# Kernel tuning notes

Measured on AMD Instinct MI355X. Metric: run time of the kernel, lower is better.

The kernel has to match this reference:

```python
import jax, jax.numpy as jnp
import numpy as np

H, W = 256, 256
N = 512


def setup_inputs() -> dict:
    key = jax.random.key(0)
    k1, k2, k3, k4, k5 = jax.random.split(key, 5)
    # gaussian centers in front of the camera
    xy = jax.random.normal(k1, (N, 2), dtype=jnp.float32) * 3.0
    z = jax.random.uniform(k2, (N,), dtype=jnp.float32, minval=2.0, maxval=45.0)
    means3D = jnp.concatenate([xy, z[:, None]], axis=1)  # (N,3)
    # SPD 3x3 covariances
    A = jax.random.normal(k3, (N, 3, 3), dtype=jnp.float32) * 0.2
    covs3d = jnp.einsum('nij,nkj->nik', A, A) + 0.05 * jnp.eye(3, dtype=jnp.float32)
    colors = jax.random.uniform(k4, (N, 3), dtype=jnp.float32)
    opacities = jax.random.uniform(k5, (N,), dtype=jnp.float32)
    K = jnp.array([[300.0, 0.0, W / 2.0], [0.0, 300.0, H / 2.0], [0.0, 0.0, 1.0]], dtype=jnp.float32)
    R = jnp.eye(3, dtype=jnp.float32)
    t = jnp.zeros((3,), dtype=jnp.float32)
    return {"means3D": means3D, "covs3d": covs3d, "colors": colors,
            "opacities": opacities, "K": K, "R": R, "t": t}


def _render(means3D, covs3d, colors, opacities, K, R, t):
    # --- projection ---
    cam = means3D @ R.T + t                       # (N,3)
    Z = cam[:, 2]                                 # raw camera-space depth
    depths = jnp.maximum(Z, 1.0)                  # clamped (used for sort/mask)
    screen = cam @ K.T
    means2D = screen[:, :2] / screen[:, 2:3]      # (N,2)
    fx, fy = K[0, 0], K[1, 1]
    zeros = jnp.zeros_like(Z)
    # Jacobian of perspective projection, (N,2,3); uses raw Z as in the original
    J = jnp.stack([
        jnp.stack([fx / Z, zeros, -fx * cam[:, 0] / (Z * Z)], axis=-1),
        jnp.stack([zeros, fy / Z, -fy * cam[:, 1] / (Z * Z)], axis=-1),
    ], axis=1)
    covs_cam = jnp.einsum('ij,njk,lk->nil', R, covs3d, R)     # R Sigma R^T
    covs2D = jnp.einsum('nij,njk,nlk->nil', J, covs_cam, J)   # J Sigma_cam J^T, (N,2,2)

    valid = (depths > 1.0) & (depths < 50.0)
    # front-to-back sort by clamped depth
    idx = jnp.argsort(depths)
    means2D = means2D[idx]
    covs2D = covs2D[idx]
    colors_s = colors[idx]
    op_s = opacities[idx]
    valid = valid[idx]

    # --- per-gaussian per-pixel density ---
    covs2D = covs2D + 1e-4 * jnp.eye(2, dtype=covs2D.dtype)
    cov_inv = jnp.linalg.inv(covs2D)              # (N,2,2)
    cov_det = jnp.linalg.det(covs2D)              # (N,)
    norm = 1.0 / (2.0 * jnp.pi * jnp.sqrt(cov_det))

    ys, xs = jnp.meshgrid(jnp.arange(H, dtype=jnp.float32),
                          jnp.arange(W, dtype=jnp.float32), indexing='ij')
    pixels = jnp.stack([xs, ys], axis=-1)         # (H,W,2), [x,y]

    dx = pixels[None] - means2D[:, None, None, :]                 # (N,H,W,2)
    expo = -0.5 * jnp.einsum('nhwi,nij,nhwj->nhw', dx, cov_inv, dx)
    gaussian = norm[:, None, None] * jnp.exp(expo)                # (N,H,W)
    gaussian = gaussian * valid.astype(gaussian.dtype)[:, None, None]

    # --- alpha compositing (inclusive cumprod as in the original) ---
    alphas = op_s[:, None, None] * gaussian                       # (N,H,W)
    T = jnp.cumprod(1.0 - alphas, axis=0)
    weights = alphas * T
    rendered = jnp.einsum('nhw,nc->hwc', weights, colors_s)       # (H,W,3)
    return rendered


def reference(means3D, covs3d, colors, opacities, K, R, t):
    return _render(means3D, covs3d, colors, opacities, K, R, t)
```

## Files before the change

### kernel.cpp

```cpp
#include <hip/hip_runtime.h>


constexpr int   REC   = 16;
constexpr int   WIMG  = 256;
constexpr int   HIMG  = 256;
constexpr int   SPLIT = 8;
constexpr float LOG2E  = 1.4426950408889634f;
constexpr float INV2PI = 0.15915494309189535f;
constexpr float INVEPS = 1.0e7f;

__global__ __launch_bounds__(512) void gs_preprocess(
    const float* __restrict__ means3D, const float* __restrict__ covs3d,
    const float* __restrict__ colors,  const float* __restrict__ opac,
    const float* __restrict__ Km,      const float* __restrict__ Rm,
    const float* __restrict__ tvec,    float* __restrict__ recs, int N)
{
    __shared__ float s_depth[512];
    __shared__ int   s_cnt[64][9];
    const int t  = threadIdx.x;
    const int l  = t & 63, p = t >> 6;
    const int gi = (int)blockIdx.x * 64 + l;

    float d_all = 3.0e38f;
    if (t < N) {
        const float m0 = means3D[t*3+0], m1 = means3D[t*3+1], m2 = means3D[t*3+2];
        d_all = fmaxf(Rm[6]*m0 + Rm[7]*m1 + Rm[8]*m2 + tvec[2], 1.0f);
    }
    s_depth[t] = d_all;
    __syncthreads();

    const float dg = s_depth[gi & 511];
    int cnt = 0;
    #pragma unroll 16
    for (int j = p*64; j < p*64 + 64; ++j) {
        const float dj = s_depth[j];
        cnt += (dj < dg) || (dj == dg && j < gi);
    }
    s_cnt[l][p] = cnt;

    float rec[13];
    const bool act = (p == 0) && (gi < N);
    if (act) {
        float Kl[9], Rl[9], tl[3];
        #pragma unroll
        for (int k = 0; k < 9; ++k) { Kl[k] = Km[k]; Rl[k] = Rm[k]; }
        tl[0] = tvec[0]; tl[1] = tvec[1]; tl[2] = tvec[2];

        const float m0 = means3D[gi*3+0], m1 = means3D[gi*3+1], m2 = means3D[gi*3+2];
        const float cam0 = Rl[0]*m0 + Rl[1]*m1 + Rl[2]*m2 + tl[0];
        const float cam1 = Rl[3]*m0 + Rl[4]*m1 + Rl[5]*m2 + tl[1];
        const float cam2 = Rl[6]*m0 + Rl[7]*m1 + Rl[8]*m2 + tl[2];
        const float Z = cam2;
        const float depth = fmaxf(Z, 1.0f);

        const float s0 = Kl[0]*cam0 + Kl[1]*cam1 + Kl[2]*cam2;
        const float s1 = Kl[3]*cam0 + Kl[4]*cam1 + Kl[5]*cam2;
        const float s2 = Kl[6]*cam0 + Kl[7]*cam1 + Kl[8]*cam2;
        const float mx = s0 / s2, my = s1 / s2;

        const float fx = Kl[0], fy = Kl[4];
        const float iz = 1.0f / Z;
        float J[2][3];
        J[0][0] = fx*iz; J[0][1] = 0.0f;  J[0][2] = -fx*cam0*iz*iz;
        J[1][0] = 0.0f;  J[1][1] = fy*iz; J[1][2] = -fy*cam1*iz*iz;

        float S[9];
        #pragma unroll
        for (int k = 0; k < 9; ++k) S[k] = covs3d[gi*9+k];

        float RS[9], Cc[9];
        #pragma unroll
        for (int r = 0; r < 3; ++r)
            #pragma unroll
            for (int c = 0; c < 3; ++c)
                RS[r*3+c] = Rl[r*3+0]*S[0+c] + Rl[r*3+1]*S[3+c] + Rl[r*3+2]*S[6+c];
        #pragma unroll
        for (int r = 0; r < 3; ++r)
            #pragma unroll
            for (int c = 0; c < 3; ++c)
                Cc[r*3+c] = RS[r*3+0]*Rl[c*3+0] + RS[r*3+1]*Rl[c*3+1] + RS[r*3+2]*Rl[c*3+2];

        float JC[2][3];
        #pragma unroll
        for (int r = 0; r < 2; ++r)
            #pragma unroll
            for (int c = 0; c < 3; ++c)
                JC[r][c] = J[r][0]*Cc[0+c] + J[r][1]*Cc[3+c] + J[r][2]*Cc[6+c];

        const float c200 = JC[0][0]*J[0][0] + JC[0][1]*J[0][1] + JC[0][2]*J[0][2] + 1e-4f;
        const float c201 = JC[0][0]*J[1][0] + JC[0][1]*J[1][1] + JC[0][2]*J[1][2];
        const float c210 = JC[1][0]*J[0][0] + JC[1][1]*J[0][1] + JC[1][2]*J[0][2];
        const float c211 = JC[1][0]*J[1][0] + JC[1][1]*J[1][1] + JC[1][2]*J[1][2] + 1e-4f;

        const float det  = c200*c211 - c201*c210;
        const float idet = 1.0f / det;
        const float ia   = c211*idet;
        const float i01  = -0.5f*(c201 + c210)*idet;
        const float ic   = c200*idet;
        const float ibs  = 2.0f*i01;

        const bool  valid = (depth > 1.0f) && (depth < 50.0f);
        const float nrm   = valid ? (INV2PI / sqrtf(det)) : 0.0f;
        const float opn   = opac[gi] * nrm;

        const float c1 = i01 / ia;
        const float c2 = ic - i01*i01/ia;
        const float L2 = 2.0f * logf(opn * INVEPS);

        rec[0]  = my;  rec[1] = c2;  rec[2] = L2;  rec[3] = c1;
        rec[4]  = mx;  rec[5] = ia;
        rec[6]  = -0.5f*LOG2E*ia;
        rec[7]  = -0.5f*LOG2E*ibs;
        rec[8]  = -0.5f*LOG2E*ic;
        rec[9]  = opn;
        rec[10] = colors[gi*3+0];
        rec[11] = colors[gi*3+1];
        rec[12] = colors[gi*3+2];
    }
    __syncthreads();

    if (act) {
        int rank = 0;
        #pragma unroll
        for (int q = 0; q < 8; ++q) rank += s_cnt[l][q];
        float4* dst = (float4*)(recs + rank*REC);
        dst[0] = make_float4(rec[0],  rec[1],  rec[2],  rec[3]);
        dst[1] = make_float4(rec[4],  rec[5],  rec[6],  rec[7]);
        dst[2] = make_float4(rec[8],  rec[9],  rec[10], rec[11]);
        dst[3] = make_float4(rec[12], 0.0f,    0.0f,    0.0f);
    }
}

__global__ __launch_bounds__(512, 8) void gs_render(
    const float* __restrict__ recs, float* __restrict__ out, int N)
{
    __shared__ float  s_my[512], s_c2[512], s_L2[512], s_c1[512], s_mx[512], s_p0[512];
    __shared__ float  s_ev[512][12];
    __shared__ float4 s_part[SPLIT][64];
    __shared__ float  s_rgb[192];

    const int t = threadIdx.x;

    if (t < N) {
        const float4 a = *(const float4*)(recs + t*REC + 0);
        const float4 b = *(const float4*)(recs + t*REC + 4);
        const float4 c = *(const float4*)(recs + t*REC + 8);
        const float4 d = *(const float4*)(recs + t*REC + 12);
        s_my[t] = a.x; s_c2[t] = a.y; s_L2[t] = a.z; s_c1[t] = a.w;
        s_mx[t] = b.x; s_p0[t] = b.y;
        float4* ev = (float4*)s_ev[t];
        ev[0] = make_float4(b.x, a.x, b.z, b.w);
        ev[1] = make_float4(c.x, c.y, c.z, c.w);
        s_ev[t][8] = d.x;
    } else {
        s_my[t] = 0.0f; s_c2[t] = 0.0f; s_L2[t] = -1e30f;
        s_c1[t] = 0.0f; s_mx[t] = 0.0f; s_p0[t] = 1.0f;
    }
    __syncthreads();

    const int w    = t >> 6;
    const int lane = t & 63;
    const float sx0 = (float)(((int)blockIdx.x & 3) * 64);
    const float scx = sx0 + 31.5f;
    const float px  = sx0 + (float)lane;
    const float py  = (float)((int)blockIdx.x >> 2);

    const int base = w * 64;
    bool hit;
    {
        const int j = base + lane;
        const float dy  = py - s_my[j];
        const float rem = fmaf(-s_c2[j], dy*dy, s_L2[j]);
        const float xc  = fmaf(-s_c1[j], dy, s_mx[j]);
        const float t1  = fmaxf(fabsf(xc - scx) - 31.5f, 0.0f);
        hit = (s_p0[j]*t1*t1 <= rem);
    }
    unsigned long long mask = __ballot(hit);

    float T = 1.0f, cr = 0.0f, cg = 0.0f, cb = 0.0f;
    while (mask) {
        const int k = __builtin_ctzll(mask);
        mask &= mask - 1;
        const float* e = s_ev[base + k];
        const float4 v0 = *(const float4*)(e + 0);
        const float4 v1 = *(const float4*)(e + 4);
        const float  bl = e[8];
        const float dx = px - v0.x;
        const float dy = py - v0.y;
        const float e2 = fmaf(v0.z, dx*dx, fmaf(v0.w, dx*dy, v1.x*dy*dy));
        const float al = v1.y * __builtin_amdgcn_exp2f(e2);
        T *= (1.0f - al);
        const float wt = al * T;
        cr = fmaf(wt, v1.z, cr);
        cg = fmaf(wt, v1.w, cg);
        cb = fmaf(wt, bl,  cb);
    }

    s_part[w][lane] = make_float4(T, cr, cg, cb);
    __syncthreads();

    if (t < 64) {
        float4 f = s_part[0][t];
        float Ta = f.x, r_ = f.y, g_ = f.z, b_ = f.w;
        #pragma unroll
        for (int k = 1; k < SPLIT; ++k) {
            const float4 p = s_part[k][t];
            r_ = fmaf(Ta, p.y, r_);
            g_ = fmaf(Ta, p.z, g_);
            b_ = fmaf(Ta, p.w, b_);
            Ta *= p.x;
        }
        s_rgb[t*3+0] = r_;
        s_rgb[t*3+1] = g_;
        s_rgb[t*3+2] = b_;
    }
    __syncthreads();

    if (t < 192) {
        out[(int)blockIdx.x * 192 + t] = s_rgb[t];
    }
}

extern "C" void kernel_launch(void* const* d_in, const int* in_sizes, int n_in,
                              void* d_out, int out_size, void* d_ws, size_t ws_size,
                              hipStream_t stream)
{
    const float* means3D = (const float*)d_in[0];
    const float* covs3d  = (const float*)d_in[1];
    const float* colors  = (const float*)d_in[2];
    const float* opac    = (const float*)d_in[3];
    const float* Km      = (const float*)d_in[4];
    const float* Rm      = (const float*)d_in[5];
    const float* tv      = (const float*)d_in[6];
    const int N = in_sizes[3];

    float* recs = (float*)d_ws;
    float* out  = (float*)d_out;

    gs_preprocess<<<dim3((N + 63) / 64), dim3(512), 0, stream>>>(
        means3D, covs3d, colors, opac, Km, Rm, tv, recs, N);

    gs_render<<<dim3(WIMG * HIMG / 64), dim3(512), 0, stream>>>(recs, out, N);
}
```

Measured before the change: 16.11 us.

## Render two pixel rows per block and compact hit lists in shared memory

Each render block now covers a 64x2 pixel tile instead of 64x1, so the per-block staging of all gaussian records into shared memory is amortised over twice as many pixels. Each thread composites two pixels and reuses one record load and the dx terms for both. The ballot/ctz loop is replaced by a compacted per-wave hit index list in shared memory. Culling is now a union over two rows, so some gaussians get evaluated for pixels they barely touch. Launch bounds occupancy hint drops from 8 to 4 and the grid is halved, which reduces parallelism.

```diff
diff --git a/kernel.cpp b/kernel.cpp
--- a/kernel.cpp
+++ b/kernel.cpp
@@ -131,13 +131,14 @@
     }
 }
 
-__global__ __launch_bounds__(512, 8) void gs_render(
+__global__ __launch_bounds__(512, 4) void gs_render(
     const float* __restrict__ recs, float* __restrict__ out, int N)
 {
     __shared__ float  s_my[512], s_c2[512], s_L2[512], s_c1[512], s_mx[512], s_p0[512];
     __shared__ float  s_ev[512][12];
-    __shared__ float4 s_part[SPLIT][64];
-    __shared__ float  s_rgb[192];
+    __shared__ int    s_hits[SPLIT][64];
+    __shared__ float4 s_part[2][SPLIT][64];
+    __shared__ float  s_rgb[2][192];
 
     const int t = threadIdx.x;
 
@@ -160,64 +161,92 @@
 
     const int w    = t >> 6;
     const int lane = t & 63;
-    const float sx0 = (float)(((int)blockIdx.x & 3) * 64);
+    const int xs   = (int)blockIdx.x & 3;
+    const int pr   = (int)blockIdx.x >> 2;
+    const float y0f = (float)(2*pr);
+    const float sx0 = (float)(xs * 64);
     const float scx = sx0 + 31.5f;
     const float px  = sx0 + (float)lane;
-    const float py  = (float)((int)blockIdx.x >> 2);
 
     const int base = w * 64;
     bool hit;
     {
         const int j = base + lane;
-        const float dy  = py - s_my[j];
-        const float rem = fmaf(-s_c2[j], dy*dy, s_L2[j]);
-        const float xc  = fmaf(-s_c1[j], dy, s_mx[j]);
-        const float t1  = fmaxf(fabsf(xc - scx) - 31.5f, 0.0f);
-        hit = (s_p0[j]*t1*t1 <= rem);
-    }
-    unsigned long long mask = __ballot(hit);
-
-    float T = 1.0f, cr = 0.0f, cg = 0.0f, cb = 0.0f;
-    while (mask) {
-        const int k = __builtin_ctzll(mask);
-        mask &= mask - 1;
-        const float* e = s_ev[base + k];
+        const float myj = s_my[j], c2 = s_c2[j], L2 = s_L2[j];
+        const float c1  = s_c1[j], mxj = s_mx[j], p0 = s_p0[j];
+        float dy  = y0f - myj;
+        float rem = fmaf(-c2, dy*dy, L2);
+        float xc  = fmaf(-c1, dy, mxj);
+        float t1  = fmaxf(fabsf(xc - scx) - 31.5f, 0.0f);
+        const bool h0 = (p0*t1*t1 <= rem);
+        dy  = dy + 1.0f;
+        rem = fmaf(-c2, dy*dy, L2);
+        xc  = xc - c1;
+        t1  = fmaxf(fabsf(xc - scx) - 31.5f, 0.0f);
+        const bool h1 = (p0*t1*t1 <= rem);
+        hit = h0 | h1;
+    }
+    const unsigned long long mask = __ballot(hit);
+    const int nhit = __popcll(mask);
+    if (hit) {
+        const int pos = __popcll(mask & ((1ull << lane) - 1ull));
+        s_hits[w][pos] = base + lane;
+    }
+
+    float T0 = 1.0f, r0 = 0.0f, g0 = 0.0f, b0 = 0.0f;
+    float T1 = 1.0f, r1 = 0.0f, g1 = 0.0f, b1 = 0.0f;
+
+    for (int i = 0; i < nhit; ++i) {
+        const int j = s_hits[w][i];
+        const float* e = s_ev[j];
         const float4 v0 = *(const float4*)(e + 0);
         const float4 v1 = *(const float4*)(e + 4);
         const float  bl = e[8];
-        const float dx = px - v0.x;
-        const float dy = py - v0.y;
-        const float e2 = fmaf(v0.z, dx*dx, fmaf(v0.w, dx*dy, v1.x*dy*dy));
-        const float al = v1.y * __builtin_amdgcn_exp2f(e2);
-        T *= (1.0f - al);
-        const float wt = al * T;
-        cr = fmaf(wt, v1.z, cr);
-        cg = fmaf(wt, v1.w, cg);
-        cb = fmaf(wt, bl,  cb);
-    }
-
-    s_part[w][lane] = make_float4(T, cr, cg, cb);
-    __syncthreads();
-
-    if (t < 64) {
-        float4 f = s_part[0][t];
+
+        const float dx   = px - v0.x;
+        const float adx2 = v0.z * dx * dx;
+        const float u    = v0.w * dx;
+        const float dy0  = y0f - v0.y;
+        const float dy1  = dy0 + 1.0f;
+        const float e20  = fmaf(dy0, fmaf(v1.x, dy0, u), adx2);
+        const float e21  = fmaf(dy1, fmaf(v1.x, dy1, u), adx2);
+        const float al0  = v1.y * __builtin_amdgcn_exp2f(e20);
+        const float al1  = v1.y * __builtin_amdgcn_exp2f(e21);
+
+        T0 *= (1.0f - al0);
+        const float w0 = al0 * T0;
+        r0 = fmaf(w0, v1.z, r0); g0 = fmaf(w0, v1.w, g0); b0 = fmaf(w0, bl, b0);
+
+        T1 *= (1.0f - al1);
+        const float w1 = al1 * T1;
+        r1 = fmaf(w1, v1.z, r1); g1 = fmaf(w1, v1.w, g1); b1 = fmaf(w1, bl, b1);
+    }
+
+    s_part[0][w][lane] = make_float4(T0, r0, g0, b0);
+    s_part[1][w][lane] = make_float4(T1, r1, g1, b1);
+    __syncthreads();
+
+    if (t < 128) {
+        const int row = t >> 6, p = t & 63;
+        float4 f = s_part[row][0][p];
         float Ta = f.x, r_ = f.y, g_ = f.z, b_ = f.w;
         #pragma unroll
         for (int k = 1; k < SPLIT; ++k) {
-            const float4 p = s_part[k][t];
-            r_ = fmaf(Ta, p.y, r_);
-            g_ = fmaf(Ta, p.z, g_);
-            b_ = fmaf(Ta, p.w, b_);
-            Ta *= p.x;
+            const float4 q = s_part[row][k][p];
+            r_ = fmaf(Ta, q.y, r_);
+            g_ = fmaf(Ta, q.z, g_);
+            b_ = fmaf(Ta, q.w, b_);
+            Ta *= q.x;
         }
-        s_rgb[t*3+0] = r_;
-        s_rgb[t*3+1] = g_;
-        s_rgb[t*3+2] = b_;
-    }
-    __syncthreads();
-
-    if (t < 192) {
-        out[(int)blockIdx.x * 192 + t] = s_rgb[t];
+        s_rgb[row][p*3+0] = r_;
+        s_rgb[row][p*3+1] = g_;
+        s_rgb[row][p*3+2] = b_;
+    }
+    __syncthreads();
+
+    if (t < 384) {
+        const int row = t / 192, i = t - row * 192;
+        out[(2*pr + row) * (WIMG*3) + xs*192 + i] = s_rgb[row][i];
     }
 }
 
@@ -240,5 +269,5 @@
     gs_preprocess<<<dim3((N + 63) / 64), dim3(512), 0, stream>>>(
         means3D, covs3d, colors, opac, Km, Rm, tv, recs, N);
 
-    gs_render<<<dim3(WIMG * HIMG / 64), dim3(512), 0, stream>>>(recs, out, N);
+    gs_render<<<dim3(WIMG * HIMG / 128), dim3(512), 0, stream>>>(recs, out, N);
 }
```

After: 15.78 us (median of 2 runs). -2.1%, faster.
